# Kernel optimization log

Measured on AMD Instinct MI355X. Metric: run time of the kernel, lower is better.

The kernel has to match this reference:

```python
import jax, jax.numpy as jnp
import numpy as np

N, L, S, H, D = 1, 4096, 4096, 8, 32


def setup_inputs() -> dict:
    key = jax.random.key(0)
    k1, k2, k3 = jax.random.split(key, 3)
    q = jax.random.normal(k1, (N, L, H, D), dtype=jnp.float32)
    k = jax.random.normal(k2, (N, S, H, D), dtype=jnp.float32)
    v = jax.random.normal(k3, (N, S, H, D), dtype=jnp.float32)
    q_mask = jnp.ones((N, L), dtype=bool)
    kv_mask = jnp.ones((N, S), dtype=bool)
    return {"q": q, "k": k, "v": v, "q_mask": q_mask, "kv_mask": kv_mask}


def reference(q, k, v, q_mask, kv_mask):
    # qk: [N, L, S, H] -- full score tensor as in the torch module
    qk = jnp.einsum('nlhd,nshd->nlsh', q, k)
    # mask BEFORE scaling (matches torch: masked_fill then divide by sqrt(D))
    mask = ~(q_mask[:, :, None, None] & kv_mask[:, None, :, None])
    qk = jnp.where(mask, jnp.float32(-1e9), qk)
    scale = q.shape[3] ** 0.5
    attn = jax.nn.softmax(qk / scale, axis=2)  # softmax over S
    out = jnp.einsum('nlsh,nshd->nlhd', attn, v)
    return out
```

## Files before the change

kernel.cpp:

```cpp
#include <hip/hip_runtime.h>
#include <hip/hip_bf16.h>

typedef __bf16 bf16x8 __attribute__((ext_vector_type(8)));
typedef float  f32x4  __attribute__((ext_vector_type(4)));

#define H_  8
#define D_  32
#define L_  4096
#define S_  4096
#define BM  64
#define BN  64
#define PSTRIDE 36

__device__ __forceinline__ int vmap(int d) { return ((d & 7) << 2) | (d >> 3); }
__device__ __forceinline__ int pmap(int m) { return ((m & 3) << 2) | (m >> 2); }

template<bool DIRECT>
__global__ __launch_bounds__(256, 8)
void fattn_main(const float* __restrict__ q, const float* __restrict__ kk,
                const float* __restrict__ v, float* __restrict__ dst, int schunk)
{
    const int qt   = blockIdx.x;
    const int h    = blockIdx.y;
    const int sp   = blockIdx.z;
    const int tid  = threadIdx.x;
    const int wave = tid >> 6;
    const int lane = tid & 63;
    const int col  = lane & 15;
    const int quad = lane >> 4;

    __shared__ __align__(16) __bf16 Ks[BN][40];
    __shared__ __align__(16) __bf16 Vt[D_][72];
    __shared__ __align__(16) __bf16 Ps[4][16][72];

    const int qrow0 = qt * BM + wave * 16 + col;
    bf16x8 qa;
    {
        const float* qp = q + ((size_t)qrow0 * H_ + h) * D_ + quad * 8;
        float4 q0 = *(const float4*)(qp);
        float4 q1 = *(const float4*)(qp + 4);
        qa[0]=(__bf16)q0.x; qa[1]=(__bf16)q0.y; qa[2]=(__bf16)q0.z; qa[3]=(__bf16)q0.w;
        qa[4]=(__bf16)q1.x; qa[5]=(__bf16)q1.y; qa[6]=(__bf16)q1.z; qa[7]=(__bf16)q1.w;
    }

    f32x4 o0 = {0,0,0,0}, o1 = {0,0,0,0};
    float lsum[4] = {0.f, 0.f, 0.f, 0.f};

    const float cs = 0.17677669529663687f * 1.4426950408889634f;

    const int srow  = tid >> 2;
    const int dseg  = (tid & 3) * 8;
    const int vbase = dseg >> 3;
    const int vrow_r0 = vmap(col);
    const int vrow_r1 = vmap(col + 16);
    const int prow_r  = pmap(col);

    const int sbeg = sp * schunk;
    const int send = sbeg + schunk;

    for (int s0 = sbeg; s0 < send; s0 += BN) {
        __syncthreads();
        {
            const size_t goff = ((size_t)(s0 + srow) * H_ + h) * D_ + dseg;
            float4 k0 = *(const float4*)(kk + goff);
            float4 k1 = *(const float4*)(kk + goff + 4);
            bf16x8 kb;
            kb[0]=(__bf16)k0.x; kb[1]=(__bf16)k0.y; kb[2]=(__bf16)k0.z; kb[3]=(__bf16)k0.w;
            kb[4]=(__bf16)k1.x; kb[5]=(__bf16)k1.y; kb[6]=(__bf16)k1.z; kb[7]=(__bf16)k1.w;
            *(bf16x8*)(&Ks[srow][dseg]) = kb;
            float4 v0 = *(const float4*)(v + goff);
            float4 v1 = *(const float4*)(v + goff + 4);
            float vv[8] = {v0.x, v0.y, v0.z, v0.w, v1.x, v1.y, v1.z, v1.w};
#pragma unroll
            for (int j = 0; j < 8; ++j)
                Vt[(j << 2) | vbase][srow] = (__bf16)vv[j];
        }
        __syncthreads();

        f32x4 sc[4];
        const f32x4 zc = {0, 0, 0, 0};
#pragma unroll
        for (int ct = 0; ct < 4; ++ct) {
            bf16x8 kb = *(const bf16x8*)(&Ks[ct * 16 + col][quad * 8]);
            sc[ct] = __builtin_amdgcn_mfma_f32_16x16x32_bf16(qa, kb, zc, 0, 0, 0);
        }

#pragma unroll
        for (int r = 0; r < 4; ++r) {
            const int prow = pmap(quad * 4 + r);
#pragma unroll
            for (int ct = 0; ct < 4; ++ct) {
                float p = __builtin_amdgcn_exp2f(sc[ct][r] * cs);
                __bf16 pb = (__bf16)p;
                Ps[wave][prow][ct * 16 + col] = pb;
                lsum[r] += (float)pb;
            }
        }

#pragma unroll
        for (int c2 = 0; c2 < 2; ++c2) {
            bf16x8 pa  = *(const bf16x8*)(&Ps[wave][prow_r][c2 * 32 + quad * 8]);
            bf16x8 vb0 = *(const bf16x8*)(&Vt[vrow_r0][c2 * 32 + quad * 8]);
            bf16x8 vb1 = *(const bf16x8*)(&Vt[vrow_r1][c2 * 32 + quad * 8]);
            o0 = __builtin_amdgcn_mfma_f32_16x16x32_bf16(pa, vb0, o0, 0, 0, 0);
            o1 = __builtin_amdgcn_mfma_f32_16x16x32_bf16(pa, vb1, o1, 0, 0, 0);
        }
    }

#pragma unroll
    for (int r = 0; r < 4; ++r) {
#pragma unroll
        for (int off = 1; off < 16; off <<= 1)
            lsum[r] += __shfl_xor(lsum[r], off);
        const int qrow = qt * BM + wave * 16 + quad * 4 + r;
        if (DIRECT) {
            float inv = 1.f / lsum[r];
            float* op = dst + ((size_t)qrow * H_ + h) * D_;
            op[col]      = o0[r] * inv;
            op[16 + col] = o1[r] * inv;
        } else {
            float* pr = dst + ((size_t)(sp * H_ + h) * L_ + qrow) * PSTRIDE;
            pr[col]      = o0[r];
            pr[16 + col] = o1[r];
            if (col == 0) pr[32] = lsum[r];
        }
    }
}

__global__ __launch_bounds__(256)
void fattn_combine(const float* __restrict__ ws, float* __restrict__ out, int nsplit)
{
    const int i = blockIdx.x * 256 + threadIdx.x;
    const int d = i & 31, h = (i >> 5) & 7, l = i >> 8;
    float num = 0.f, den = 0.f;
    for (int sp = 0; sp < nsplit; ++sp) {
        const float* pr = ws + ((size_t)(sp * H_ + h) * L_ + l) * PSTRIDE;
        num += pr[d];
        den += pr[32];
    }
    out[i] = num / den;
}

extern "C" void kernel_launch(void* const* d_in, const int* in_sizes, int n_in,
                              void* d_out, int out_size, void* d_ws, size_t ws_size,
                              hipStream_t stream) {
    const float* q = (const float*)d_in[0];
    const float* k = (const float*)d_in[1];
    const float* v = (const float*)d_in[2];
    float* out = (float*)d_out;
    const int NSPLIT = 4;
    size_t need = (size_t)NSPLIT * H_ * L_ * PSTRIDE * sizeof(float);
    if (ws_size >= need) {
        fattn_main<false><<<dim3(L_ / BM, H_, NSPLIT), 256, 0, stream>>>(
            q, k, v, (float*)d_ws, S_ / NSPLIT);
        fattn_combine<<<dim3((L_ * H_ * D_) / 256), 256, 0, stream>>>(
            (const float*)d_ws, out, NSPLIT);
    } else {
        fattn_main<true><<<dim3(L_ / BM, H_, 1), 256, 0, stream>>>(q, k, v, out, S_);
    }
}
```

Before: 127.7 us.

## Compute transposed scores to keep P in registers and fold row sums into MFMA

Computes S^T = K·Q^T so each lane's exponentiated scores already match the B-operand layout of a 16x16x16 MFMA. This removes the shared-memory round trip for P and the per-tile softmax stores. Row sums now come from an extra MFMA against a ones vector, which replaces the scalar adds and the final shuffle reduction. V is stored transposed with an XOR swizzle, and the split workspace is reorganised into contiguous num/den arrays so the combine step can use vectorised loads and stores. In exchange, the PV step issues more, smaller MFMAs (K=16 instead of K=32), plus one extra MFMA per tile for the sum.

```diff
diff --git a/kernel.cpp b/kernel.cpp
--- a/kernel.cpp
+++ b/kernel.cpp
@@ -1,6 +1,7 @@
 #include <hip/hip_runtime.h>
 #include <hip/hip_bf16.h>
 
+typedef __bf16 bf16x4 __attribute__((ext_vector_type(4)));
 typedef __bf16 bf16x8 __attribute__((ext_vector_type(8)));
 typedef float  f32x4  __attribute__((ext_vector_type(4)));
 
@@ -10,54 +11,55 @@
 #define S_  4096
 #define BM  64
 #define BN  64
-#define PSTRIDE 36
+#define NSPLIT 4
 
-__device__ __forceinline__ int vmap(int d) { return ((d & 7) << 2) | (d >> 3); }
-__device__ __forceinline__ int pmap(int m) { return ((m & 3) << 2) | (m >> 2); }
+static __device__ __forceinline__ f32x4 mfma_k16(bf16x4 a, bf16x4 b, f32x4 c) {
+#if __has_builtin(__builtin_amdgcn_mfma_f32_16x16x16_bf16)
+    return __builtin_amdgcn_mfma_f32_16x16x16_bf16(a, b, c, 0, 0, 0);
+#elif __has_builtin(__builtin_amdgcn_mfma_f32_16x16x16bf16_1k)
+    typedef short s16x4 __attribute__((ext_vector_type(4)));
+    union U { bf16x4 h; s16x4 s; };
+    U ua, ub; ua.h = a; ub.h = b;
+    return __builtin_amdgcn_mfma_f32_16x16x16bf16_1k(ua.s, ub.s, c, 0, 0, 0);
+#else
+    asm("v_mfma_f32_16x16x16_bf16 %0, %1, %2, %0" : "+v"(c) : "v"(a), "v"(b));
+    return c;
+#endif
+}
 
 template<bool DIRECT>
 __global__ __launch_bounds__(256, 8)
 void fattn_main(const float* __restrict__ q, const float* __restrict__ kk,
-                const float* __restrict__ v, float* __restrict__ dst, int schunk)
+                const float* __restrict__ v, float* __restrict__ num,
+                float* __restrict__ den, float* __restrict__ out, int schunk)
 {
-    const int qt   = blockIdx.x;
-    const int h    = blockIdx.y;
-    const int sp   = blockIdx.z;
-    const int tid  = threadIdx.x;
-    const int wave = tid >> 6;
-    const int lane = tid & 63;
-    const int col  = lane & 15;
-    const int quad = lane >> 4;
+    const int qt = blockIdx.x, h = blockIdx.y, sp = blockIdx.z;
+    const int tid = threadIdx.x, wave = tid >> 6, lane = tid & 63;
+    const int col = lane & 15, quad = lane >> 4;
 
     __shared__ __align__(16) __bf16 Ks[BN][40];
     __shared__ __align__(16) __bf16 Vt[D_][72];
-    __shared__ __align__(16) __bf16 Ps[4][16][72];
 
-    const int qrow0 = qt * BM + wave * 16 + col;
-    bf16x8 qa;
+    const int qn = qt * BM + wave * 16 + col;
+    bf16x8 qb;
     {
-        const float* qp = q + ((size_t)qrow0 * H_ + h) * D_ + quad * 8;
-        float4 q0 = *(const float4*)(qp);
+        const float* qp = q + ((size_t)qn * H_ + h) * D_ + quad * 8;
+        float4 q0 = *(const float4*)qp;
         float4 q1 = *(const float4*)(qp + 4);
-        qa[0]=(__bf16)q0.x; qa[1]=(__bf16)q0.y; qa[2]=(__bf16)q0.z; qa[3]=(__bf16)q0.w;
-        qa[4]=(__bf16)q1.x; qa[5]=(__bf16)q1.y; qa[6]=(__bf16)q1.z; qa[7]=(__bf16)q1.w;
+        qb[0]=(__bf16)q0.x; qb[1]=(__bf16)q0.y; qb[2]=(__bf16)q0.z; qb[3]=(__bf16)q0.w;
+        qb[4]=(__bf16)q1.x; qb[5]=(__bf16)q1.y; qb[6]=(__bf16)q1.z; qb[7]=(__bf16)q1.w;
     }
 
-    f32x4 o0 = {0,0,0,0}, o1 = {0,0,0,0};
-    float lsum[4] = {0.f, 0.f, 0.f, 0.f};
-
+    f32x4 o0 = {0,0,0,0}, o1 = {0,0,0,0}, accl = {0,0,0,0};
+    const f32x4 zc = {0,0,0,0};
+    const bf16x4 ones = {(__bf16)1.f, (__bf16)1.f, (__bf16)1.f, (__bf16)1.f};
     const float cs = 0.17677669529663687f * 1.4426950408889634f;
 
-    const int srow  = tid >> 2;
-    const int dseg  = (tid & 3) * 8;
-    const int vbase = dseg >> 3;
-    const int vrow_r0 = vmap(col);
-    const int vrow_r1 = vmap(col + 16);
-    const int prow_r  = pmap(col);
+    const int srow = tid >> 2;
+    const int dseg = (tid & 3) * 8;
+    const int vsw  = (col & 7) << 2;
 
-    const int sbeg = sp * schunk;
-    const int send = sbeg + schunk;
-
+    const int sbeg = sp * schunk, send = sbeg + schunk;
     for (int s0 = sbeg; s0 < send; s0 += BN) {
         __syncthreads();
         {
@@ -72,73 +74,64 @@
             float4 v1 = *(const float4*)(v + goff + 4);
             float vv[8] = {v0.x, v0.y, v0.z, v0.w, v1.x, v1.y, v1.z, v1.w};
 #pragma unroll
-            for (int j = 0; j < 8; ++j)
-                Vt[(j << 2) | vbase][srow] = (__bf16)vv[j];
+            for (int j = 0; j < 8; ++j) {
+                const int d = dseg + j;
+                Vt[d][srow ^ ((d & 7) << 2)] = (__bf16)vv[j];
+            }
         }
         __syncthreads();
 
-        f32x4 sc[4];
-        const f32x4 zc = {0, 0, 0, 0};
 #pragma unroll
-        for (int ct = 0; ct < 4; ++ct) {
-            bf16x8 kb = *(const bf16x8*)(&Ks[ct * 16 + col][quad * 8]);
-            sc[ct] = __builtin_amdgcn_mfma_f32_16x16x32_bf16(qa, kb, zc, 0, 0, 0);
-        }
-
+        for (int sb = 0; sb < 4; ++sb) {
+            bf16x8 ka = *(const bf16x8*)(&Ks[sb * 16 + col][quad * 8]);
+            f32x4 st = __builtin_amdgcn_mfma_f32_16x16x32_bf16(ka, qb, zc, 0, 0, 0);
+            bf16x4 pb;
 #pragma unroll
-        for (int r = 0; r < 4; ++r) {
-            const int prow = pmap(quad * 4 + r);
-#pragma unroll
-            for (int ct = 0; ct < 4; ++ct) {
-                float p = __builtin_amdgcn_exp2f(sc[ct][r] * cs);
-                __bf16 pb = (__bf16)p;
-                Ps[wave][prow][ct * 16 + col] = pb;
-                lsum[r] += (float)pb;
-            }
-        }
-
-#pragma unroll
-        for (int c2 = 0; c2 < 2; ++c2) {
-            bf16x8 pa  = *(const bf16x8*)(&Ps[wave][prow_r][c2 * 32 + quad * 8]);
-            bf16x8 vb0 = *(const bf16x8*)(&Vt[vrow_r0][c2 * 32 + quad * 8]);
-            bf16x8 vb1 = *(const bf16x8*)(&Vt[vrow_r1][c2 * 32 + quad * 8]);
-            o0 = __builtin_amdgcn_mfma_f32_16x16x32_bf16(pa, vb0, o0, 0, 0, 0);
-            o1 = __builtin_amdgcn_mfma_f32_16x16x32_bf16(pa, vb1, o1, 0, 0, 0);
+            for (int r = 0; r < 4; ++r)
+                pb[r] = (__bf16)__builtin_amdgcn_exp2f(st[r] * cs);
+            const int sco = (sb * 16 + quad * 4) ^ vsw;
+            bf16x4 va0 = *(const bf16x4*)(&Vt[col][sco]);
+            bf16x4 va1 = *(const bf16x4*)(&Vt[col + 16][sco]);
+            o0   = mfma_k16(va0,  pb, o0);
+            o1   = mfma_k16(va1,  pb, o1);
+            accl = mfma_k16(ones, pb, accl);
         }
     }
 
-#pragma unroll
-    for (int r = 0; r < 4; ++r) {
-#pragma unroll
-        for (int off = 1; off < 16; off <<= 1)
-            lsum[r] += __shfl_xor(lsum[r], off);
-        const int qrow = qt * BM + wave * 16 + quad * 4 + r;
-        if (DIRECT) {
-            float inv = 1.f / lsum[r];
-            float* op = dst + ((size_t)qrow * H_ + h) * D_;
-            op[col]      = o0[r] * inv;
-            op[16 + col] = o1[r] * inv;
-        } else {
-            float* pr = dst + ((size_t)(sp * H_ + h) * L_ + qrow) * PSTRIDE;
-            pr[col]      = o0[r];
-            pr[16 + col] = o1[r];
-            if (col == 0) pr[32] = lsum[r];
-        }
+    if (DIRECT) {
+        const float inv = 1.f / accl[0];
+        float* op = out + ((size_t)qn * H_ + h) * D_;
+        f32x4 r0 = {o0[0]*inv, o0[1]*inv, o0[2]*inv, o0[3]*inv};
+        f32x4 r1 = {o1[0]*inv, o1[1]*inv, o1[2]*inv, o1[3]*inv};
+        *(f32x4*)(op + quad * 4)      = r0;
+        *(f32x4*)(op + 16 + quad * 4) = r1;
+    } else {
+        float* pr = num + (((size_t)(sp * H_ + h) * L_ + qn) << 5);
+        *(f32x4*)(pr + quad * 4)      = o0;
+        *(f32x4*)(pr + 16 + quad * 4) = o1;
+        if (quad == 0) den[(size_t)(sp * H_ + h) * L_ + qn] = accl[0];
     }
 }
 
 __global__ __launch_bounds__(256)
-void fattn_combine(const float* __restrict__ ws, float* __restrict__ out, int nsplit)
+void fattn_combine(const float* __restrict__ num, const float* __restrict__ den,
+                   float* __restrict__ out)
 {
-    const int i = blockIdx.x * 256 + threadIdx.x;
-    const int d = i & 31, h = (i >> 5) & 7, l = i >> 8;
-    float num = 0.f, den = 0.f;
-    for (int sp = 0; sp < nsplit; ++sp) {
-        const float* pr = ws + ((size_t)(sp * H_ + h) * L_ + l) * PSTRIDE;
-        num += pr[d];
-        den += pr[32];
+    const int i  = blockIdx.x * 256 + threadIdx.x;
+    const int d4 = (i & 7) * 4;
+    const int h  = (i >> 3) & 7;
+    const int l  = i >> 6;
+    f32x4 acc = {0,0,0,0};
+    float dn = 0.f;
+    for (int sp = 0; sp < NSPLIT; ++sp) {
+        const float* pr = num + (((size_t)(sp * H_ + h) * L_ + l) << 5) + d4;
+        f32x4 t = *(const f32x4*)pr;
+        acc[0] += t[0]; acc[1] += t[1]; acc[2] += t[2]; acc[3] += t[3];
+        dn += den[(size_t)(sp * H_ + h) * L_ + l];
     }
-    out[i] = num / den;
+    const float inv = 1.f / dn;
+    f32x4 r = {acc[0]*inv, acc[1]*inv, acc[2]*inv, acc[3]*inv};
+    *(f32x4*)(out + ((size_t)l * H_ + h) * D_ + d4) = r;
 }
 
 extern "C" void kernel_launch(void* const* d_in, const int* in_sizes, int n_in,
@@ -148,14 +141,16 @@
     const float* k = (const float*)d_in[1];
     const float* v = (const float*)d_in[2];
     float* out = (float*)d_out;
-    const int NSPLIT = 4;
-    size_t need = (size_t)NSPLIT * H_ * L_ * PSTRIDE * sizeof(float);
-    if (ws_size >= need) {
+    const size_t nnum = (size_t)NSPLIT * H_ * L_ * 32;
+    const size_t nden = (size_t)NSPLIT * H_ * L_;
+    if (ws_size >= (nnum + nden) * sizeof(float)) {
+        float* num = (float*)d_ws;
+        float* den = num + nnum;
         fattn_main<false><<<dim3(L_ / BM, H_, NSPLIT), 256, 0, stream>>>(
-            q, k, v, (float*)d_ws, S_ / NSPLIT);
-        fattn_combine<<<dim3((L_ * H_ * D_) / 256), 256, 0, stream>>>(
-            (const float*)d_ws, out, NSPLIT);
+            q, k, v, num, den, out, S_ / NSPLIT);
+        fattn_combine<<<dim3((L_ * H_ * D_ / 4) / 256), 256, 0, stream>>>(num, den, out);
     } else {
-        fattn_main<true><<<dim3(L_ / BM, H_, 1), 256, 0, stream>>>(q, k, v, out, S_);
+        fattn_main<true><<<dim3(L_ / BM, H_, 1), 256, 0, stream>>>(
+            q, k, v, nullptr, nullptr, out, S_);
     }
 }
```

Measured after the change: 119.4 us. 1.07x faster.
